# Optimization experiments

Hardware: AMD Instinct MI355X
Metric: run time of the kernel (lower is better)

## Reference

```python
import jax, jax.numpy as jnp
import numpy as np

B, S, T = 64, 49, 32
ENC, HID, EMB, VOCAB = 512, 512, 512, 32000
ATT = HID  # attention_dim = hidden_size in __init__


def setup_inputs() -> dict:
    key = jax.random.key(0)
    ks = jax.random.split(key, 20)
    def lin(k, out_d, in_d):
        s = 1.0 / np.sqrt(in_d)
        kw, kb = jax.random.split(k)
        return (jax.random.uniform(kw, (out_d, in_d), jnp.float32, -s, s),
                jax.random.uniform(kb, (out_d,), jnp.float32, -s, s))
    W_ih, b_ih = lin(ks[0], 3 * HID, EMB + ENC)
    W_hh, b_hh = lin(ks[1], 3 * HID, HID)
    W_out, b_out = lin(ks[2], VOCAB, HID)
    W_init, b_init = lin(ks[3], HID, ENC)
    W_beta, b_beta = lin(ks[4], ENC, HID)
    W_ea, b_ea = lin(ks[5], ATT, ENC)
    W_da, b_da = lin(ks[6], ATT, HID)
    W_fa, b_fa = lin(ks[7], 1, ATT)
    emb = jax.random.normal(ks[8], (VOCAB, EMB), jnp.float32)
    feats = jax.random.normal(ks[9], (B, S, ENC), jnp.float32)
    seq = jax.random.randint(ks[10], (B, T), 0, VOCAB)
    length = jax.random.randint(ks[11], (B,), 1, T + 1).at[0].set(T)
    return dict(feats=feats, seq=seq, length=length, emb=emb,
                W_ih=W_ih, b_ih=b_ih, W_hh=W_hh, b_hh=b_hh,
                W_out=W_out, b_out=b_out, W_init=W_init, b_init=b_init,
                W_beta=W_beta, b_beta=b_beta, W_ea=W_ea, b_ea=b_ea,
                W_da=W_da, b_da=b_da, W_fa=W_fa, b_fa=b_fa)


def _forward(feats, seq, length, emb, W_ih, b_ih, W_hh, b_hh, W_out, b_out,
             W_init, b_init, W_beta, b_beta, W_ea, b_ea, W_da, b_da, W_fa, b_fa):
    Tlen = seq.shape[1]
    embed_seq = emb[seq]                      # [B, T, EMB]
    embed_seq = jnp.swapaxes(embed_seq, 0, 1)  # [T, B, EMB]
    # active[t, b] = (length[b] > t); equivalent to torch's sorted shrinking batch
    active = (jnp.arange(Tlen)[:, None] < length[None, :])  # [T, B] bool
    h0 = jnp.mean(feats, axis=1) @ W_init.T + b_init         # [B, HID]
    scope0 = jnp.ones(feats.shape[:2], feats.dtype)          # [B, S]
    att1 = feats @ W_ea.T + b_ea                              # [B, S, ATT], hoisted

    def gru_cell(x, h):
        gi = x @ W_ih.T + b_ih
        gh = h @ W_hh.T + b_hh
        ir, iz, inn = jnp.split(gi, 3, axis=1)
        hr, hz, hn = jnp.split(gh, 3, axis=1)
        r = jax.nn.sigmoid(ir + hr)
        z = jax.nn.sigmoid(iz + hz)
        n = jnp.tanh(inn + r * hn)
        return (1.0 - z) * n + z * h

    def step(carry, xs):
        h, scope = carry
        embed_t, act = xs                     # [B, EMB], [B] bool
        actf = act[:, None].astype(h.dtype)
        att2 = h @ W_da.T + b_da              # [B, ATT]
        att = (jax.nn.relu(att1 + att2[:, None, :]) @ W_fa.T).squeeze(-1) + b_fa  # [B, S]
        alpha = jax.nn.softmax(att, axis=1)
        alpha_tilde = scope * alpha
        scope = jnp.where(act[:, None], scope * (1.0 - alpha), scope)
        awe = jnp.einsum('bse,bs->be', feats, alpha)          # [B, ENC]
        gate = jax.nn.sigmoid(h @ W_beta.T + b_beta)
        x = jnp.concatenate([embed_t, gate * awe], axis=1)
        h_new = gru_cell(x, h)
        h = jnp.where(act[:, None], h_new, h)
        preds = h_new @ W_out.T + b_out
        out_t = preds * actf
        alpha_out = alpha_tilde * actf
        return (h, scope), (out_t, alpha_out)

    (_, _), (output, alphas) = jax.lax.scan(step, (h0, scope0), (embed_seq, active))
    output = jnp.swapaxes(output, 0, 1)   # [B, T, VOCAB]
    alphas = jnp.swapaxes(alphas, 0, 1)   # [B, T, S]
    return output, alphas


def reference(feats, seq, length, emb, W_ih, b_ih, W_hh, b_hh, W_out, b_out,
              W_init, b_init, W_beta, b_beta, W_ea, b_ea, W_da, b_da, W_fa, b_fa):
    return _forward(feats, seq, length, emb, W_ih, b_ih, W_hh, b_hh, W_out, b_out,
                    W_init, b_init, W_beta, b_beta, W_ea, b_ea, W_da, b_da, W_fa, b_fa)
```

## Files before the change

kernel.cpp:

```cpp
#include <hip/hip_runtime.h>
#include <cstdint>
#include <cstddef>

#define B_   64
#define S_   49
#define T_   32
#define D_   512
#define V_   32000
#define G3   1536
#define NBLK 64

typedef float v4f   __attribute__((ext_vector_type(4)));
typedef int   i32x4 __attribute__((ext_vector_type(4)));
typedef _Float16 f16;
typedef _Float16 f16x8 __attribute__((ext_vector_type(8)));
typedef _Float16 f16x4 __attribute__((ext_vector_type(4)));

__device__ __forceinline__ float sigm(float x) { return 1.f / (1.f + __expf(-x)); }

__device__ __forceinline__ uint64_t ld_a64(const void* p) {
  return __hip_atomic_load((const uint64_t*)p, __ATOMIC_RELAXED, __HIP_MEMORY_SCOPE_AGENT);
}
__device__ __forceinline__ void st_a64(void* p, uint64_t v) {
  __hip_atomic_store((uint64_t*)p, v, __ATOMIC_RELAXED, __HIP_MEMORY_SCOPE_AGENT);
}
__device__ __forceinline__ uint32_t ld_a32(const void* p) {
  return __hip_atomic_load((const uint32_t*)p, __ATOMIC_RELAXED, __HIP_MEMORY_SCOPE_AGENT);
}
__device__ __forceinline__ void st_a32(void* p, uint32_t v) {
  __hip_atomic_store((uint32_t*)p, v, __ATOMIC_RELAXED, __HIP_MEMORY_SCOPE_AGENT);
}

__device__ __forceinline__ void cvt8(const float* __restrict__ in,
                                     f16* __restrict__ out) {
  float4 a = *(const float4*)in;
  float4 b = *(const float4*)(in + 4);
  f16x8 o;
  o[0] = (f16)a.x; o[1] = (f16)a.y; o[2] = (f16)a.z; o[3] = (f16)a.w;
  o[4] = (f16)b.x; o[5] = (f16)b.y; o[6] = (f16)b.z; o[7] = (f16)b.w;
  *(f16x8*)out = o;
}

__global__ __launch_bounds__(256) void k_prep(
    const float* __restrict__ Wout, f16* __restrict__ Woutb,
    const float* __restrict__ Wea, f16* __restrict__ Wea16,
    const float* __restrict__ feats, f16* __restrict__ feats16,
    const float* __restrict__ emb, const int* __restrict__ seq,
    const int* __restrict__ length,
    f16* __restrict__ xemb16, float* __restrict__ actmask,
    float* __restrict__ hmean) {
  const size_t N1 = (size_t)V_ * D_ / 8;
  const size_t N2 = N1 + (size_t)D_ * D_ / 8;
  const size_t N3 = N2 + (size_t)B_ * S_ * D_ / 8;
  const size_t N4 = N3 + (size_t)B_ * T_ * D_ / 8;
  const size_t N5 = N4 + (size_t)B_ * D_;
  const size_t N6 = N5 + (size_t)B_ * T_;
  for (size_t i = (size_t)blockIdx.x * 256 + threadIdx.x; i < N6;
       i += (size_t)gridDim.x * 256) {
    if (i < N1) {
      cvt8(Wout + i * 8, Woutb + i * 8);
    } else if (i < N2) {
      size_t j = i - N1;
      cvt8(Wea + j * 8, Wea16 + j * 8);
    } else if (i < N3) {
      size_t j = i - N2;
      cvt8(feats + j * 8, feats16 + j * 8);
    } else if (i < N4) {
      size_t j = i - N3;
      int m = (int)(j >> 6), c = (int)(j & 63);
      int t = m >> 6, b = m & 63;
      int idx = seq[b * T_ + t];
      cvt8(emb + (size_t)idx * D_ + c * 8, xemb16 + (size_t)m * D_ + c * 8);
    } else if (i < N5) {
      size_t j = i - N4;
      int b = (int)(j >> 9), e = (int)(j & 511);
      float s = 0.f;
      for (int si = 0; si < S_; ++si)
        s += feats[((size_t)b * S_ + si) * D_ + e];
      hmean[b * D_ + e] = s * (1.f / 49.f);
    } else {
      size_t j = i - N5;
      int b = (int)(j >> 5), t = (int)(j & 31);
      actmask[b * T_ + t] = (t < length[b]) ? 1.f : 0.f;
    }
  }
}

__global__ __launch_bounds__(256) void k_gemm_f32(
    float* __restrict__ C, f16* __restrict__ C16,
    const float* __restrict__ X, const float* __restrict__ W,
    const float* __restrict__ bias, int N, int K, int ldw) {
  __shared__ __align__(16) float XsT[32][68];
  __shared__ __align__(16) float WsT[32][68];
  const int nbase = blockIdx.x * 64, mbase = blockIdx.y * 64;
  const int tid = threadIdx.x;
  const int lr = tid >> 2;
  const int lk = (tid & 3) * 8;
  const int ty = tid >> 4, tx = tid & 15;
  float acc[4][4] = {};
  for (int k0 = 0; k0 < K; k0 += 32) {
    {
      const float* xs = X + (size_t)(mbase + lr) * K + k0 + lk;
      const float* wsrc = W + (size_t)(nbase + lr) * ldw + k0 + lk;
      float4 x0 = *(const float4*)xs, x1 = *(const float4*)(xs + 4);
      float4 w0 = *(const float4*)wsrc, w1 = *(const float4*)(wsrc + 4);
      XsT[lk + 0][lr] = x0.x; XsT[lk + 1][lr] = x0.y; XsT[lk + 2][lr] = x0.z; XsT[lk + 3][lr] = x0.w;
      XsT[lk + 4][lr] = x1.x; XsT[lk + 5][lr] = x1.y; XsT[lk + 6][lr] = x1.z; XsT[lk + 7][lr] = x1.w;
      WsT[lk + 0][lr] = w0.x; WsT[lk + 1][lr] = w0.y; WsT[lk + 2][lr] = w0.z; WsT[lk + 3][lr] = w0.w;
      WsT[lk + 4][lr] = w1.x; WsT[lk + 5][lr] = w1.y; WsT[lk + 6][lr] = w1.z; WsT[lk + 7][lr] = w1.w;
    }
    __syncthreads();
    #pragma unroll
    for (int kk = 0; kk < 32; ++kk) {
      float4 a4 = *(const float4*)&XsT[kk][ty * 4];
      float4 w4 = *(const float4*)&WsT[kk][tx * 4];
      float av[4] = {a4.x, a4.y, a4.z, a4.w};
      float wv[4] = {w4.x, w4.y, w4.z, w4.w};
      #pragma unroll
      for (int i = 0; i < 4; ++i)
        #pragma unroll
        for (int j = 0; j < 4; ++j)
          acc[i][j] = fmaf(av[i], wv[j], acc[i][j]);
    }
    __syncthreads();
  }
  #pragma unroll
  for (int i = 0; i < 4; ++i) {
    int m = mbase + ty * 4 + i;
    int n = nbase + tx * 4;
    float4 o;
    o.x = acc[i][0] + bias[n + 0];
    o.y = acc[i][1] + bias[n + 1];
    o.z = acc[i][2] + bias[n + 2];
    o.w = acc[i][3] + bias[n + 3];
    *(float4*)&C[(size_t)m * N + n] = o;
    if (C16) {
      f16x4 h;
      h[0] = (f16)o.x; h[1] = (f16)o.y; h[2] = (f16)o.z; h[3] = (f16)o.w;
      *(f16x4*)&C16[(size_t)m * N + n] = h;
    }
  }
}

#define GEMM16_CORE                                                            \
  __shared__ __align__(16) f16 As[128 * 32];                                   \
  __shared__ __align__(16) f16 Bs[128 * 32];                                   \
  const int tid = threadIdx.x;                                                 \
  const int l = tid & 63, w = tid >> 6;                                        \
  const int wr = w >> 1, wc = w & 1;                                           \
  const int lm = l & 15;                                                       \
  const int kc = l >> 4;                                                       \
  const int rchunk = (kc ^ ((lm >> 1) & 3)) * 8;                               \
  v4f acc[4][4];                                                               \
  _Pragma("unroll")                                                            \
  for (int mi = 0; mi < 4; ++mi)                                               \
    _Pragma("unroll")                                                          \
    for (int ni = 0; ni < 4; ++ni)                                             \
      acc[mi][ni] = (v4f){0.f, 0.f, 0.f, 0.f};                                 \
  i32x4 ra[2], rb[2];                                                          \
  auto LD = [&](int k0) {                                                      \
    _Pragma("unroll")                                                          \
    for (int i = 0; i < 2; ++i) {                                              \
      int ch = i * 256 + tid;                                                  \
      int row = ch >> 2, cq = ch & 3;                                          \
      ra[i] = *(const i32x4*)&A[(size_t)(mb + row) * 512 + k0 + cq * 8];       \
      rb[i] = *(const i32x4*)&Bw[(size_t)(nb + row) * 512 + k0 + cq * 8];      \
    }                                                                          \
  };                                                                           \
  LD(0);                                                                       \
  for (int k0 = 0; k0 < 512; k0 += 32) {                                       \
    _Pragma("unroll")                                                          \
    for (int i = 0; i < 2; ++i) {                                              \
      int ch = i * 256 + tid;                                                  \
      int row = ch >> 2, cq = ch & 3;                                          \
      int sc = (cq ^ ((row >> 1) & 3)) * 8;                                    \
      *(i32x4*)&As[row * 32 + sc] = ra[i];                                     \
      *(i32x4*)&Bs[row * 32 + sc] = rb[i];                                     \
    }                                                                          \
    __syncthreads();                                                           \
    if (k0 < 480) LD(k0 + 32);                                                 \
    f16x8 af[4], bf[4];                                                        \
    _Pragma("unroll")                                                          \
    for (int mi = 0; mi < 4; ++mi)                                             \
      af[mi] = *(const f16x8*)&As[(wr * 64 + mi * 16 + lm) * 32 + rchunk];     \
    _Pragma("unroll")                                                          \
    for (int ni = 0; ni < 4; ++ni)                                             \
      bf[ni] = *(const f16x8*)&Bs[(wc * 64 + ni * 16 + lm) * 32 + rchunk];     \
    _Pragma("unroll")                                                          \
    for (int mi = 0; mi < 4; ++mi)                                             \
      _Pragma("unroll")                                                        \
      for (int ni = 0; ni < 4; ++ni)                                           \
        acc[mi][ni] = __builtin_amdgcn_mfma_f32_16x16x32_f16(af[mi], bf[ni], acc[mi][ni], 0, 0, 0); \
    __syncthreads();                                                           \
  }

__global__ __launch_bounds__(256) void k_gemm16f(
    const f16* __restrict__ A, const f16* __restrict__ Bw,
    const float* __restrict__ bias, f16* __restrict__ out) {
  const int nb = blockIdx.x * 128, mb = blockIdx.y * 128;
  GEMM16_CORE
  #pragma unroll
  for (int ni = 0; ni < 4; ++ni) {
    int n = nb + wc * 64 + ni * 16 + lm;
    float bo = bias[n];
    #pragma unroll
    for (int mi = 0; mi < 4; ++mi) {
      int m0 = mb + wr * 64 + mi * 16 + (l >> 4) * 4;
      #pragma unroll
      for (int r = 0; r < 4; ++r) {
        int m = m0 + r;
        if (m < B_ * S_) out[(size_t)m * 512 + n] = (f16)(acc[mi][ni][r] + bo);
      }
    }
  }
}

__global__ __launch_bounds__(256) void k_gemm16g(
    const f16* __restrict__ A, const f16* __restrict__ Bw,
    const float* __restrict__ bias, float* __restrict__ out) {
  const int nb = blockIdx.x * 128, mb = blockIdx.y * 128;
  GEMM16_CORE
  #pragma unroll
  for (int ni = 0; ni < 4; ++ni) {
    int n = nb + wc * 64 + ni * 16 + lm;
    float bo = bias[n];
    int gate = n >> 9, rem = n & 511;
    int Kb = rem >> 3, jl = rem & 7;
    #pragma unroll
    for (int mi = 0; mi < 4; ++mi) {
      int m0 = mb + wr * 64 + mi * 16 + (l >> 4) * 4;
      int t = m0 >> 6, b0q = m0 & 63;
      float* dst = out + (((size_t)t * 64 + Kb) * 32 + gate * 8 + jl) * 64 + b0q;
      #pragma unroll
      for (int r = 0; r < 4; ++r)
        dst[r] = acc[mi][ni][r] + bo;
    }
  }
}

__global__ __launch_bounds__(256) void k_packW(
    const float* __restrict__ Wda, const float* __restrict__ Wbe,
    const float* __restrict__ Whh, const float* __restrict__ Wih,
    f16* __restrict__ Wp1, f16* __restrict__ Wp2, f16* __restrict__ Wp3) {
  int K = blockIdx.x, tid = threadIdx.x;
  for (int idx = tid; idx < 40 * 512; idx += 256) {
    int r = idx >> 9, e = idx & 511;
    float v;
    if (r < 8)       v = Wda[(size_t)(8 * K + r) * D_ + e];
    else if (r < 16) v = Wbe[(size_t)(8 * K + r - 8) * D_ + e];
    else if (r < 24) v = Whh[(size_t)(8 * K + r - 16) * D_ + e];
    else if (r < 32) v = Whh[(size_t)(512 + 8 * K + r - 24) * D_ + e];
    else             v = Whh[(size_t)(1024 + 8 * K + r - 32) * D_ + e];
    Wp1[(size_t)K * 20480 + idx] = (f16)v;
  }
  for (int idx = tid; idx < 24 * 512; idx += 256) {
    int r = idx >> 9, e = idx & 511;
    int g = r >> 3, jj = r & 7;
    float v = Wih[(size_t)(g * 512 + 8 * K + jj) * 1024 + 512 + e];
    Wp2[(size_t)K * 12288 + idx] = (f16)v;
  }
  for (int idx = tid; idx < 24 * 512; idx += 256) {
    int rl = idx >> 9, e = idx & 511;
    int r = K * 24 + rl;
    Wp3[(size_t)r * 512 + e] = (f16)Wih[(size_t)r * 1024 + e];
  }
}

__device__ __forceinline__ void wait_flags64(const int* __restrict__ flags,
                                             int target, int tid) {
  if (tid < 64) {
    while (!__all((int)ld_a32(flags + tid * 16) >= target)) {}
  }
  __syncthreads();
}

__device__ __forceinline__ void set_flag(int* slot, int val, int tid) {
  __syncthreads();
  if (tid == 0) st_a32(slot, (uint32_t)val);
}

__device__ __forceinline__ void stage_fast(const f16* __restrict__ src,
                                           uint4* __restrict__ hs, int tid) {
  const i32x4* s = (const i32x4*)src;
  i32x4 v[16];
  #pragma unroll
  for (int i = 0; i < 16; ++i) {
    asm volatile("global_load_dwordx4 %0, %1, off sc0 sc1"
                 : "=v"(v[i]) : "v"(s + i * 256 + tid));
  }
  asm volatile("s_waitcnt vmcnt(0)" ::: "memory");
  __builtin_amdgcn_sched_barrier(0);
  #pragma unroll
  for (int i = 0; i < 16; ++i) {
    int g = i * 256 + tid;
    int b = g >> 6, c = g & 63;
    *(i32x4*)&hs[b * 64 + (c ^ (b & 7))] = v[i];
  }
}

__global__ __launch_bounds__(256, 1) void k_recur(
    const f16* __restrict__ Wp1, const f16* __restrict__ Wp2,
    const f16* __restrict__ att116, const f16* __restrict__ feats16,
    const float* __restrict__ gi_pack,
    const float* __restrict__ b_da, const float* __restrict__ b_beta,
    const float* __restrict__ b_hh,
    const float* __restrict__ W_fa, const float* __restrict__ b_fa,
    const int* __restrict__ length,
    f16* __restrict__ h16, f16* __restrict__ xg16,
    float* __restrict__ att2g,
    float* __restrict__ alphas, f16* __restrict__ Hbuf,
    int* __restrict__ flags) {
  __shared__ __align__(16) uint4 lds_all[8704];
  __shared__ float gh_lds[24 * 72];
  __shared__ float gix_lds[24 * 72];
  __shared__ float att2_s[512];
  __shared__ float gate_s[512];
  __shared__ float att_s[64];
  __shared__ float alpha_s[64];
  uint4* hs = lds_all;
  uint4* W1 = lds_all + 4096;
  uint4* W2 = lds_all + 6656;
  float* attp = (float*)(lds_all + 8192);

  const int K = blockIdx.x, tid = threadIdx.x;
  const int w = tid >> 6, l = tid & 63;
  const int lm = l & 15, c4 = l >> 4;
  const int bq = tid & 63, jg = tid >> 6;
  const int jj0 = 2 * jg, jj1 = 2 * jg + 1;
  int* flagA = flags;
  int* flagB = flags + 1024;
  int* flagC = flags + 2048;

  {
    const uint4* s1 = (const uint4*)(Wp1 + (size_t)K * 20480);
    const uint4* s2 = (const uint4*)(Wp2 + (size_t)K * 12288);
    #pragma unroll
    for (int i = 0; i < 10; ++i) {
      int g = i * 256 + tid;
      int s = g >> 6, c = g & 63;
      W1[s * 64 + (c ^ (s & 7))] = s1[g];
    }
    #pragma unroll
    for (int i = 0; i < 6; ++i) {
      int g = i * 256 + tid;
      int s = g >> 6, c = g & 63;
      W2[s * 64 + (c ^ (s & 7))] = s2[g];
    }
  }
  const int lenB = length[K];
  const float bfa0 = b_fa[0];
  const int lb = length[bq];
  const float bhr0 = b_hh[8 * K + jj0],        bhr1 = b_hh[8 * K + jj1];
  const float bhz0 = b_hh[512 + 8 * K + jj0],  bhz1 = b_hh[512 + 8 * K + jj1];
  const float bhn0 = b_hh[1024 + 8 * K + jj0], bhn1 = b_hh[1024 + 8 * K + jj1];
  float wfa[8];
  {
    int a0i = l * 8;
    #pragma unroll
    for (int jx = 0; jx < 8; ++jx) wfa[jx] = W_fa[a0i + jx];
  }
  const float bda0 = b_da[2 * tid], bda1 = b_da[2 * tid + 1];
  const float bbe0 = b_beta[2 * tid], bbe1 = b_beta[2 * tid + 1];
  float scope_r = 1.f;
  __syncthreads();

  for (int t = 0; t < T_; ++t) {
    if (t) wait_flags64(flagC, t, tid);
    stage_fast(h16, hs, tid);
    __syncthreads();
    float hold0, hold1;
    {
      f16x8 hv = __builtin_bit_cast(f16x8, hs[bq * 64 + (K ^ (bq & 7))]);
      hold0 = (float)hv[jj0]; hold1 = (float)hv[jj1];
    }
    {
      v4f a0 = {0.f, 0.f, 0.f, 0.f};
      int bb = w * 16 + lm;
      #pragma unroll
      for (int kt = 0; kt < 16; ++kt) {
        int ca = kt * 4 + c4;
        f16x8 av = __builtin_bit_cast(f16x8, hs[bb * 64 + (ca ^ (bb & 7))]);
        f16x8 b0 = __builtin_bit_cast(f16x8, W1[lm * 64 + (ca ^ (lm & 7))]);
        a0 = __builtin_amdgcn_mfma_f32_16x16x32_f16(av, b0, a0, 0, 0, 0);
      }
      #pragma unroll
      for (int r = 0; r < 4; ++r)
        attp[(w * 16 + c4 * 4 + r) * 16 + lm] = a0[r];
    }
    __syncthreads();
    #pragma unroll
    for (int q = 0; q < 2; ++q) {
      int pp = tid * 2 + q;
      int bat = pp >> 3, pi = pp & 7;
      float2 f2;
      f2.x = attp[bat * 16 + 2 * pi];
      f2.y = attp[bat * 16 + 2 * pi + 1];
      size_t idx = (size_t)bat * 512 +
                   ((pi < 4) ? (4 * K + pi) : (256 + 4 * K + (pi - 4)));
      st_a64((uint64_t*)att2g + idx, __builtin_bit_cast(uint64_t, f2));
    }
    set_flag(flagA + K * 16, t + 1, tid);
    i32x4 attv[13];
    #pragma unroll
    for (int i = 0; i < 13; ++i) {
      int s = w + 4 * i;
      if (s < S_)
        attv[i] = *(const i32x4*)(att116 + ((size_t)K * S_ + s) * D_ + l * 8);
    }
    {
      v4f a1 = {0.f, 0.f, 0.f, 0.f};
      int bb = w * 16 + lm;
      #pragma unroll
      for (int kt = 0; kt < 16; ++kt) {
        int ca = kt * 4 + c4;
        f16x8 av = __builtin_bit_cast(f16x8, hs[bb * 64 + (ca ^ (bb & 7))]);
        f16x8 b1 = __builtin_bit_cast(f16x8, W1[(16 + lm) * 64 + (ca ^ ((16 + lm) & 7))]);
        a1 = __builtin_amdgcn_mfma_f32_16x16x32_f16(av, b1, a1, 0, 0, 0);
      }
      #pragma unroll
      for (int r = 0; r < 4; ++r)
        gh_lds[lm * 72 + (w * 16 + c4 * 4 + r)] = a1[r];
    }
    wait_flags64(flagA, t + 1, tid);
    {
      bool act = t < lenB;
      const uint64_t* arow2 = (const uint64_t*)att2g + (size_t)K * 512;
      {
        float2 f = __builtin_bit_cast(float2, ld_a64(arow2 + tid));
        att2_s[2 * tid]     = f.x + bda0;
        att2_s[2 * tid + 1] = f.y + bda1;
        float2 g = __builtin_bit_cast(float2, ld_a64(arow2 + tid + 256));
        gate_s[2 * tid]     = sigm(g.x + bbe0);
        gate_s[2 * tid + 1] = sigm(g.y + bbe1);
      }
      __syncthreads();
      int a0i = l * 8;
      #pragma unroll
      for (int i = 0; i < 13; ++i) {
        int s = w + 4 * i;
        if (s < S_) {
          f16x8 av = __builtin_bit_cast(f16x8, attv[i]);
          float p = 0.f;
          #pragma unroll
          for (int jx = 0; jx < 8; ++jx) {
            float v = (float)av[jx] + att2_s[a0i + jx];
            v = v > 0.f ? v : 0.f;
            p = fmaf(v, wfa[jx], p);
          }
          #pragma unroll
          for (int off = 32; off > 0; off >>= 1) p += __shfl_xor(p, off, 64);
          if (l == 0) att_s[s] = p + bfa0;
        }
      }
      __syncthreads();
      if (tid < 64) {
        float x = (tid < S_) ? att_s[tid] : -1e30f;
        float m = x;
        #pragma unroll
        for (int off = 32; off > 0; off >>= 1) m = fmaxf(m, __shfl_xor(m, off, 64));
        float e = (tid < S_) ? __expf(x - m) : 0.f;
        float su = e;
        #pragma unroll
        for (int off = 32; off > 0; off >>= 1) su += __shfl_xor(su, off, 64);
        if (tid < S_) alpha_s[tid] = e / su;
      }
      __syncthreads();
      if (tid < S_) {
        float al = alpha_s[tid];
        alphas[((size_t)K * T_ + t) * S_ + tid] = act ? scope_r * al : 0.f;
        scope_r = act ? scope_r * (1.f - al) : scope_r;
      }
      if (tid < 128) {
        int e0 = tid * 4;
        float s0 = 0.f, s1 = 0.f, s2 = 0.f, s3 = 0.f;
        #pragma unroll 7
        for (int s = 0; s < S_; ++s) {
          float al = alpha_s[s];
          f16x4 fv = *(const f16x4*)(feats16 + ((size_t)K * S_ + s) * D_ + e0);
          s0 = fmaf(al, (float)fv[0], s0);
          s1 = fmaf(al, (float)fv[1], s1);
          s2 = fmaf(al, (float)fv[2], s2);
          s3 = fmaf(al, (float)fv[3], s3);
        }
        f16x4 o;
        o[0] = (f16)(gate_s[e0 + 0] * s0);
        o[1] = (f16)(gate_s[e0 + 1] * s1);
        o[2] = (f16)(gate_s[e0 + 2] * s2);
        o[3] = (f16)(gate_s[e0 + 3] * s3);
        st_a64((uint64_t*)xg16 + (size_t)K * 128 + tid,
               __builtin_bit_cast(uint64_t, o));
      }
    }
    set_flag(flagB + K * 16, t + 1, tid);
    {
      v4f a2 = {0.f, 0.f, 0.f, 0.f};
      int bb = w * 16 + lm;
      #pragma unroll
      for (int kt = 0; kt < 16; ++kt) {
        int ca = kt * 4 + c4;
        f16x8 av = __builtin_bit_cast(f16x8, hs[bb * 64 + (ca ^ (bb & 7))]);
        f16x8 b2 = __builtin_bit_cast(f16x8, W1[(32 + lm) * 64 + (ca ^ ((32 + lm) & 7))]);
        a2 = __builtin_amdgcn_mfma_f32_16x16x32_f16(av, b2, a2, 0, 0, 0);
      }
      #pragma unroll
      for (int r = 0; r < 4; ++r)
        if (lm < 8) gh_lds[(16 + lm) * 72 + (w * 16 + c4 * 4 + r)] = a2[r];
    }
    wait_flags64(flagB, t + 1, tid);
    stage_fast(xg16, hs, tid);
    __syncthreads();
    {
      v4f c0 = {0.f,0.f,0.f,0.f}, c1 = {0.f,0.f,0.f,0.f};
      int bb = w * 16 + lm;
      #pragma unroll
      for (int kt = 0; kt < 16; ++kt) {
        int ca = kt * 4 + c4;
        f16x8 av = __builtin_bit_cast(f16x8, hs[bb * 64 + (ca ^ (bb & 7))]);
        f16x8 b0 = __builtin_bit_cast(f16x8, W2[lm * 64 + (ca ^ (lm & 7))]);
        f16x8 b1 = __builtin_bit_cast(f16x8, W2[(16 + lm) * 64 + (ca ^ ((16 + lm) & 7))]);
        c0 = __builtin_amdgcn_mfma_f32_16x16x32_f16(av, b0, c0, 0, 0, 0);
        c1 = __builtin_amdgcn_mfma_f32_16x16x32_f16(av, b1, c1, 0, 0, 0);
      }
      #pragma unroll
      for (int r = 0; r < 4; ++r) {
        int bat = w * 16 + c4 * 4 + r;
        gix_lds[lm * 72 + bat] = c0[r];
        if (lm < 8) gix_lds[(16 + lm) * 72 + bat] = c1[r];
      }
    }
    __syncthreads();
    {
      const float* gp = gi_pack + (size_t)(t * 64 + K) * 2048;
      float r0 = sigm(gix_lds[jj0 * 72 + bq] + gp[jj0 * 64 + bq] + gh_lds[jj0 * 72 + bq] + bhr0);
      float r1 = sigm(gix_lds[jj1 * 72 + bq] + gp[jj1 * 64 + bq] + gh_lds[jj1 * 72 + bq] + bhr1);
      float z0 = sigm(gix_lds[(8 + jj0) * 72 + bq] + gp[(8 + jj0) * 64 + bq] + gh_lds[(8 + jj0) * 72 + bq] + bhz0);
      float z1 = sigm(gix_lds[(8 + jj1) * 72 + bq] + gp[(8 + jj1) * 64 + bq] + gh_lds[(8 + jj1) * 72 + bq] + bhz1);
      float n0 = tanhf(gix_lds[(16 + jj0) * 72 + bq] + gp[(16 + jj0) * 64 + bq] + r0 * (gh_lds[(16 + jj0) * 72 + bq] + bhn0));
      float n1 = tanhf(gix_lds[(16 + jj1) * 72 + bq] + gp[(16 + jj1) * 64 + bq] + r1 * (gh_lds[(16 + jj1) * 72 + bq] + bhn1));
      float hn0 = (1.f - z0) * n0 + z0 * hold0;
      float hn1 = (1.f - z1) * n1 + z1 * hold1;
      bool act = t < lb;
      unsigned short u0 = __builtin_bit_cast(unsigned short, (f16)(act ? hn0 : hold0));
      unsigned short u1 = __builtin_bit_cast(unsigned short, (f16)(act ? hn1 : hold1));
      st_a32((uint32_t*)h16 + bq * 256 + 4 * K + jg,
             (uint32_t)u0 | ((uint32_t)u1 << 16));
      unsigned short p0 = __builtin_bit_cast(unsigned short, (f16)hn0);
      unsigned short p1 = __builtin_bit_cast(unsigned short, (f16)hn1);
      ((uint32_t*)Hbuf)[((size_t)bq * T_ + t) * 256 + 4 * K + jg] =
          (uint32_t)p0 | ((uint32_t)p1 << 16);
    }
    set_flag(flagC + K * 16, t + 1, tid);
  }
}

__global__ __launch_bounds__(256) void k_outgemm(
    const f16* __restrict__ A, const f16* __restrict__ Bw,
    const float* __restrict__ b_out, const float* __restrict__ actmask,
    float* __restrict__ out) {
  const int bid = blockIdx.x;
  const int swz = (bid & 7) * 500 + (bid >> 3);
  const int mb = (swz & 15) * 128;
  const int nb = (swz >> 4) * 128;
  GEMM16_CORE
  #pragma unroll
  for (int ni = 0; ni < 4; ++ni) {
    int n = nb + wc * 64 + ni * 16 + lm;
    float bo = b_out[n];
    #pragma unroll
    for (int mi = 0; mi < 4; ++mi) {
      int m0 = mb + wr * 64 + mi * 16 + (l >> 4) * 4;
      #pragma unroll
      for (int r = 0; r < 4; ++r) {
        int m = m0 + r;
        out[(size_t)m * V_ + n] = actmask[m] * (acc[mi][ni][r] + bo);
      }
    }
  }
}

extern "C" void kernel_launch(void* const* d_in, const int* in_sizes, int n_in,
                              void* d_out, int out_size, void* d_ws, size_t ws_size,
                              hipStream_t stream) {
  const float* feats  = (const float*)d_in[0];
  const int*   seq    = (const int*)d_in[1];
  const int*   length = (const int*)d_in[2];
  const float* emb    = (const float*)d_in[3];
  const float* W_ih   = (const float*)d_in[4];
  const float* b_ih   = (const float*)d_in[5];
  const float* W_hh   = (const float*)d_in[6];
  const float* b_hh   = (const float*)d_in[7];
  const float* W_out  = (const float*)d_in[8];
  const float* b_out  = (const float*)d_in[9];
  const float* W_init = (const float*)d_in[10];
  const float* b_init = (const float*)d_in[11];
  const float* W_beta = (const float*)d_in[12];
  const float* b_beta = (const float*)d_in[13];
  const float* W_ea   = (const float*)d_in[14];
  const float* b_ea   = (const float*)d_in[15];
  const float* W_da   = (const float*)d_in[16];
  const float* b_da   = (const float*)d_in[17];
  const float* W_fa   = (const float*)d_in[18];
  const float* b_fa   = (const float*)d_in[19];

  float* out    = (float*)d_out;
  float* alphas = out + (size_t)B_ * T_ * V_;

  float* ws = (float*)d_ws;
  int*   flags    = (int*)ws;        ws += 4096;
  float* h0       = ws;              ws += B_ * D_;
  float* hmean    = ws;              ws += B_ * D_;
  float* actmask  = ws;              ws += B_ * T_;
  float* att2g    = ws;              ws += B_ * 1024;
  float* gi_pack  = ws;              ws += (size_t)T_ * 64 * 32 * 64;
  f16* fp = (f16*)ws;
  f16* Woutb   = fp;  fp += (size_t)V_ * D_;
  f16* Hbuf    = fp;  fp += (size_t)B_ * T_ * D_;
  f16* Wp1     = fp;  fp += (size_t)64 * 20480;
  f16* Wp2     = fp;  fp += (size_t)64 * 12288;
  f16* Wp3     = fp;  fp += (size_t)G3 * D_;
  f16* Wea16   = fp;  fp += (size_t)D_ * D_;
  f16* xemb16  = fp;  fp += (size_t)B_ * T_ * D_;
  f16* feats16 = fp;  fp += (size_t)3200 * D_;
  f16* att116  = fp;  fp += (size_t)B_ * S_ * D_;
  f16* h16     = fp;  fp += B_ * D_;
  f16* xg16    = fp;  fp += B_ * D_;

  hipMemsetAsync(flags, 0, 16384, stream);

  k_prep<<<2048, 256, 0, stream>>>(W_out, Woutb, W_ea, Wea16, feats, feats16,
                                   emb, seq, length, xemb16, actmask, hmean);
  k_packW<<<64, 256, 0, stream>>>(W_da, W_beta, W_hh, W_ih, Wp1, Wp2, Wp3);
  k_gemm_f32<<<dim3(8, 1), 256, 0, stream>>>(h0, h16, hmean, W_init, b_init, 512, 512, 512);
  k_gemm16f<<<dim3(4, 25), 256, 0, stream>>>(feats16, Wea16, b_ea, att116);
  k_gemm16g<<<dim3(12, 16), 256, 0, stream>>>(xemb16, Wp3, b_ih, gi_pack);

  k_recur<<<NBLK, 256, 0, stream>>>(Wp1, Wp2, att116, feats16, gi_pack,
      b_da, b_beta, b_hh, W_fa, b_fa, length,
      h16, xg16, att2g, alphas, Hbuf, flags);

  k_outgemm<<<4000, 256, 0, stream>>>(Hbuf, Woutb, b_out, actmask, out);
}
```

Measured before the change: 910.5 us.

## Overlap W_out fp16 conversion with recurrence and double-buffer output GEMM

The fp32-to-fp16 conversion of the large W_out matrix moves out of the prep kernel into 192 extra blocks of the recurrent kernel. Those blocks convert the weights while the 64 recurrence blocks run their latency-bound sequential loop, so the conversion should no longer sit on the critical path. The output GEMM also replaces the shared core macro with an explicit double-buffered LDS pipeline that prefetches the next K-slice into registers while computing the current one. The risk is that the extra blocks compete for bandwidth or compute units with the flag-synchronized recurrence blocks.

```diff
diff --git a/kernel.cpp b/kernel.cpp
--- a/kernel.cpp
+++ b/kernel.cpp
@@ -8,7 +8,7 @@
 #define D_   512
 #define V_   32000
 #define G3   1536
-#define NBLK 64
+#define NBLK 256
 
 typedef float v4f   __attribute__((ext_vector_type(4)));
 typedef int   i32x4 __attribute__((ext_vector_type(4)));
@@ -42,26 +42,21 @@
 }
 
 __global__ __launch_bounds__(256) void k_prep(
-    const float* __restrict__ Wout, f16* __restrict__ Woutb,
     const float* __restrict__ Wea, f16* __restrict__ Wea16,
     const float* __restrict__ feats, f16* __restrict__ feats16,
     const float* __restrict__ emb, const int* __restrict__ seq,
     const int* __restrict__ length,
     f16* __restrict__ xemb16, float* __restrict__ actmask,
     float* __restrict__ hmean) {
-  const size_t N1 = (size_t)V_ * D_ / 8;
-  const size_t N2 = N1 + (size_t)D_ * D_ / 8;
+  const size_t N2 = (size_t)D_ * D_ / 8;
   const size_t N3 = N2 + (size_t)B_ * S_ * D_ / 8;
   const size_t N4 = N3 + (size_t)B_ * T_ * D_ / 8;
   const size_t N5 = N4 + (size_t)B_ * D_;
   const size_t N6 = N5 + (size_t)B_ * T_;
   for (size_t i = (size_t)blockIdx.x * 256 + threadIdx.x; i < N6;
        i += (size_t)gridDim.x * 256) {
-    if (i < N1) {
-      cvt8(Wout + i * 8, Woutb + i * 8);
-    } else if (i < N2) {
-      size_t j = i - N1;
-      cvt8(Wea + j * 8, Wea16 + j * 8);
+    if (i < N2) {
+      cvt8(Wea + i * 8, Wea16 + i * 8);
     } else if (i < N3) {
       size_t j = i - N2;
       cvt8(feats + j * 8, feats16 + j * 8);
@@ -309,6 +304,7 @@
     f16* __restrict__ h16, f16* __restrict__ xg16,
     float* __restrict__ att2g,
     float* __restrict__ alphas, f16* __restrict__ Hbuf,
+    const float* __restrict__ Wout, f16* __restrict__ Woutb,
     int* __restrict__ flags) {
   __shared__ __align__(16) uint4 lds_all[8704];
   __shared__ float gh_lds[24 * 72];
@@ -323,6 +319,14 @@
   float* attp = (float*)(lds_all + 8192);
 
   const int K = blockIdx.x, tid = threadIdx.x;
+
+  if (K >= 64) {
+    const size_t NC = (size_t)V_ * D_ / 8;
+    for (size_t i = (size_t)(K - 64) * 256 + tid; i < NC; i += (size_t)192 * 256)
+      cvt8(Wout + i * 8, Woutb + i * 8);
+    return;
+  }
+
   const int w = tid >> 6, l = tid & 63;
   const int lm = l & 15, c4 = l >> 4;
   const int bq = tid & 63, jg = tid >> 6;
@@ -557,11 +561,66 @@
     const f16* __restrict__ A, const f16* __restrict__ Bw,
     const float* __restrict__ b_out, const float* __restrict__ actmask,
     float* __restrict__ out) {
+  __shared__ __align__(16) f16 As[2][128 * 32];
+  __shared__ __align__(16) f16 Bs[2][128 * 32];
   const int bid = blockIdx.x;
   const int swz = (bid & 7) * 500 + (bid >> 3);
   const int mb = (swz & 15) * 128;
   const int nb = (swz >> 4) * 128;
-  GEMM16_CORE
+  const int tid = threadIdx.x;
+  const int l = tid & 63, w = tid >> 6;
+  const int wr = w >> 1, wc = w & 1;
+  const int lm = l & 15;
+  const int kc = l >> 4;
+  const int rchunk = (kc ^ ((lm >> 1) & 3)) * 8;
+  v4f acc[4][4];
+  #pragma unroll
+  for (int mi = 0; mi < 4; ++mi)
+    #pragma unroll
+    for (int ni = 0; ni < 4; ++ni)
+      acc[mi][ni] = (v4f){0.f, 0.f, 0.f, 0.f};
+  i32x4 ra[2], rb[2];
+  const int ch0 = tid, ch1 = 256 + tid;
+  const int row0 = ch0 >> 2, cq0 = ch0 & 3;
+  const int row1 = ch1 >> 2, cq1 = ch1 & 3;
+  const int sc0 = (cq0 ^ ((row0 >> 1) & 3)) * 8;
+  const int sc1 = (cq1 ^ ((row1 >> 1) & 3)) * 8;
+  auto LD = [&](int k0) {
+    ra[0] = *(const i32x4*)&A[(size_t)(mb + row0) * 512 + k0 + cq0 * 8];
+    rb[0] = *(const i32x4*)&Bw[(size_t)(nb + row0) * 512 + k0 + cq0 * 8];
+    ra[1] = *(const i32x4*)&A[(size_t)(mb + row1) * 512 + k0 + cq1 * 8];
+    rb[1] = *(const i32x4*)&Bw[(size_t)(nb + row1) * 512 + k0 + cq1 * 8];
+  };
+  auto ST = [&](int buf) {
+    *(i32x4*)&As[buf][row0 * 32 + sc0] = ra[0];
+    *(i32x4*)&Bs[buf][row0 * 32 + sc0] = rb[0];
+    *(i32x4*)&As[buf][row1 * 32 + sc1] = ra[1];
+    *(i32x4*)&Bs[buf][row1 * 32 + sc1] = rb[1];
+  };
+  LD(0);
+  ST(0);
+  __syncthreads();
+  int cur = 0;
+  for (int k0 = 0; k0 < 512; k0 += 32) {
+    if (k0 < 480) LD(k0 + 32);
+    f16x8 af[4], bf[4];
+    #pragma unroll
+    for (int mi = 0; mi < 4; ++mi)
+      af[mi] = *(const f16x8*)&As[cur][(wr * 64 + mi * 16 + lm) * 32 + rchunk];
+    #pragma unroll
+    for (int ni = 0; ni < 4; ++ni)
+      bf[ni] = *(const f16x8*)&Bs[cur][(wc * 64 + ni * 16 + lm) * 32 + rchunk];
+    #pragma unroll
+    for (int mi = 0; mi < 4; ++mi)
+      #pragma unroll
+      for (int ni = 0; ni < 4; ++ni)
+        acc[mi][ni] = __builtin_amdgcn_mfma_f32_16x16x32_f16(af[mi], bf[ni], acc[mi][ni], 0, 0, 0);
+    if (k0 < 480) {
+      ST(cur ^ 1);
+      __syncthreads();
+      cur ^= 1;
+    }
+  }
   #pragma unroll
   for (int ni = 0; ni < 4; ++ni) {
     int n = nb + wc * 64 + ni * 16 + lm;
@@ -627,7 +686,7 @@
 
   hipMemsetAsync(flags, 0, 16384, stream);
 
-  k_prep<<<2048, 256, 0, stream>>>(W_out, Woutb, W_ea, Wea16, feats, feats16,
+  k_prep<<<2048, 256, 0, stream>>>(W_ea, Wea16, feats, feats16,
                                    emb, seq, length, xemb16, actmask, hmean);
   k_packW<<<64, 256, 0, stream>>>(W_da, W_beta, W_hh, W_ih, Wp1, Wp2, Wp3);
   k_gemm_f32<<<dim3(8, 1), 256, 0, stream>>>(h0, h16, hmean, W_init, b_init, 512, 512, 512);
@@ -636,7 +695,7 @@
 
   k_recur<<<NBLK, 256, 0, stream>>>(Wp1, Wp2, att116, feats16, gi_pack,
       b_da, b_beta, b_hh, W_fa, b_fa, length,
-      h16, xg16, att2g, alphas, Hbuf, flags);
+      h16, xg16, att2g, alphas, Hbuf, W_out, Woutb, flags);
 
   k_outgemm<<<4000, 256, 0, stream>>>(Hbuf, Woutb, b_out, actmask, out);
 }
```

After: 916.8 us. About the same (+0.7%).
